# Optimization experiments

Measured on AMD Instinct MI355X. Metric: run time of the kernel, lower is better.

Reference implementation:

```python
import jax, jax.numpy as jnp
import numpy as np

C = 1024
HEADS = 8
HEAD_DIM = C // HEADS
SCALE = HEAD_DIM ** -0.5
GROUPS = 32
EPS = 1e-5


def _conv3(x, w, b):
    # 3x3x3 conv, padding=1 (SAME), NCDHW
    y = jax.lax.conv_general_dilated(x, w, (1, 1, 1), 'SAME',
                                     dimension_numbers=('NCDHW', 'OIDHW', 'NCDHW'))
    return y + b[None, :, None, None, None]


def _proj(x, w, b):
    # 1x1x1 conv == channel matmul; w: (C_out, C_in)
    return jnp.einsum('oc,bcdhw->bodhw', w, x) + b[None, :, None, None, None]


def _gn(x, g, b):
    B, Ch, D, H, W = x.shape
    xr = x.reshape(B, GROUPS, Ch // GROUPS, D, H, W)
    mu = xr.mean(axis=(2, 3, 4, 5), keepdims=True)
    var = xr.var(axis=(2, 3, 4, 5), keepdims=True)
    xn = ((xr - mu) * jax.lax.rsqrt(var + EPS)).reshape(B, Ch, D, H, W)
    return xn * g[None, :, None, None, None] + b[None, :, None, None, None]


def _attn(q, k, v):
    # q,k,v: (B,C,D,H,W) -> heads over channels, tokens over flattened spatial
    B, Ch, D, H, W = q.shape
    S = D * H * W
    q = q.reshape(B, HEADS, HEAD_DIM, S)
    k = k.reshape(B, HEADS, HEAD_DIM, S)
    v = v.reshape(B, HEADS, HEAD_DIM, S)
    logits = jnp.einsum('bhds,bhdt->bhst', q, k) * SCALE  # (B,H,S,S)
    a = jax.nn.softmax(logits, axis=-1)
    o = jnp.einsum('bhst,bhdt->bhds', a, v)
    return o.reshape(B, Ch, D, H, W)


def setup_inputs() -> dict:
    key = jax.random.key(0)
    ks = iter(jax.random.split(key, 40))
    def w(shape, s=0.02):
        return jax.random.normal(next(ks), shape, dtype=jnp.float32) * s
    B, D, H, W = 2, 8, 16, 16
    inp = {'x': jax.random.normal(next(ks), (B, C, D, H, W), dtype=jnp.float32)}
    for side in ('l', 'r'):
        inp[f'conv_{side}_w'] = w((C, C, 3, 3, 3))
        inp[f'conv_{side}_b'] = jnp.zeros((C,), jnp.float32)
        inp[f'gn_{side}_g'] = jnp.ones((C,), jnp.float32)
        inp[f'gn_{side}_b'] = jnp.zeros((C,), jnp.float32)
    for name in ('ql', 'kr', 'vr', 'qr', 'kl', 'vl'):
        inp[f'{name}_w'] = w((C, C))
        inp[f'{name}_b'] = jnp.zeros((C,), jnp.float32)
    inp['fus_w'] = w((C, C))
    inp['fus_b'] = jnp.zeros((C,), jnp.float32)
    inp['gn_f_g'] = jnp.ones((C,), jnp.float32)
    inp['gn_f_b'] = jnp.zeros((C,), jnp.float32)
    return inp


def reference(x, conv_l_w, conv_l_b, gn_l_g, gn_l_b,
              conv_r_w, conv_r_b, gn_r_g, gn_r_b,
              ql_w, ql_b, kr_w, kr_b, vr_w, vr_b,
              qr_w, qr_b, kl_w, kl_b, vl_w, vl_b,
              fus_w, fus_b, gn_f_g, gn_f_b):
    W = x.shape[-1]
    mid = W // 2
    x_left = x[..., :mid]
    x_right = x[..., mid:2 * mid]
    f_l = jax.nn.relu(_gn(_conv3(x_left, conv_l_w, conv_l_b), gn_l_g, gn_l_b))
    f_r = jax.nn.relu(_gn(_conv3(x_right, conv_r_w, conv_r_b), gn_r_g, gn_r_b))
    rf = jnp.flip(f_r, axis=-1)
    # left attends to flipped right
    out_l = _attn(_proj(f_l, ql_w, ql_b), _proj(rf, kr_w, kr_b), _proj(rf, vr_w, vr_b))
    # flipped right attends to left
    out_r = _attn(_proj(rf, qr_w, qr_b), _proj(f_l, kl_w, kl_b), _proj(f_l, vl_w, vl_b))
    asym_map = jnp.abs(f_l - rf).mean(axis=1, keepdims=True)
    out_r = jnp.flip(out_r, axis=-1)
    f_concat = jnp.concatenate([out_l, out_r], axis=-1)  # W even -> no pad needed
    fused = jax.nn.relu(_gn(_proj(f_concat, fus_w, fus_b), gn_f_g, gn_f_b))
    return fused, asym_map
```

## Files before the change

### kernel.cpp

```cpp
#include <hip/hip_runtime.h>
#include <hip/hip_bf16.h>
#include <stdint.h>


using bf16_t = __bf16;
using bf16x4 = __attribute__((ext_vector_type(4))) __bf16;
using bf16x8 = __attribute__((ext_vector_type(8))) __bf16;
using f32x4  = __attribute__((ext_vector_type(4))) float;

typedef const uint32_t __attribute__((address_space(1)))* gas1_t;
typedef uint32_t __attribute__((address_space(3)))* las3_t;

__device__ __forceinline__ f32x4 mfma16(bf16x8 a, bf16x8 b, f32x4 c) {
  return __builtin_amdgcn_mfma_f32_16x16x32_bf16(a, b, c, 0, 0, 0);
}
__device__ __forceinline__ void gload_lds16(const void* g, void* l) {
  __builtin_amdgcn_global_load_lds((gas1_t)g, (las3_t)l, 16, 0, 0);
}

__global__ __launch_bounds__(256) void convw_kernel(
    const float* __restrict__ wl, const float* __restrict__ wr,
    bf16_t* __restrict__ Wb)
{
  const int chunk = blockIdx.x;
  const int co    = blockIdx.y;
  const int side  = blockIdx.z;
  const float* __restrict__ src = (side ? wr : wl) + (size_t)co * 27648 + (size_t)chunk * 6912;
  __shared__ float L[6912];
  __shared__ bf16_t Lb[27][260];
  const int tid = threadIdx.x;
  for (int i = tid; i < 1728; i += 256)
    *(float4*)&L[i << 2] = *(const float4*)&src[i << 2];
  __syncthreads();
  {
    const int ci = tid;
#pragma unroll
    for (int t = 0; t < 27; ++t)
      Lb[t][ci] = (bf16_t)L[ci * 27 + t];
  }
  __syncthreads();
  bf16_t* __restrict__ dst = Wb + (size_t)side * (1024u * 27648u) + (size_t)co * 27648 + (chunk << 8);
  for (int u = tid; u < 864; u += 256) {
    const int t = u >> 5, c8 = (u & 31) << 3;
    const bf16x8 v = *(const bf16x8*)&Lb[t][c8];
    *(bf16x8*)&dst[(t << 10) + c8] = v;
  }
}

__global__ __launch_bounds__(256) void projw_kernel(
    const float* ql, const float* kl, const float* kr, const float* qr,
    const float* vl, const float* vr, const float* fu,
    bf16_t* __restrict__ Wp, float qs)
{
  const int z = blockIdx.y;
  const float* src; float s = 1.f;
  switch (z) {
    case 0: src = ql; s = qs; break;
    case 1: src = kl; break;
    case 2: src = kr; break;
    case 3: src = qr; s = qs; break;
    case 4: src = vl; break;
    case 5: src = vr; break;
    default: src = fu; break;
  }
  const size_t i4 = ((size_t)blockIdx.x * 256 + threadIdx.x) * 4;
  const float4 v = *(const float4*)(src + i4);
  bf16x4 o;
  o[0] = (bf16_t)(v.x * s); o[1] = (bf16_t)(v.y * s);
  o[2] = (bf16_t)(v.z * s); o[3] = (bf16_t)(v.w * s);
  *(bf16x4*)(Wp + (size_t)z * 1048576 + i4) = o;
}

__global__ __launch_bounds__(256) void xp_build_kernel(
    const float* __restrict__ x, bf16_t* __restrict__ Xp)
{
  const int cc0  = blockIdx.x << 6;
  const int d    = blockIdx.y;
  const int sb   = blockIdx.z;
  const int side = sb >> 1, b = sb & 1;
  __shared__ bf16_t Tls[64][132];
  const int tid = threadIdx.x;
#pragma unroll
  for (int j = 0; j < 8; ++j) {
    const int u = tid + (j << 8);
    const int ci = u >> 5, sub = u & 31;
    const int hh = sub >> 1, half = sub & 1;
    const float4 v = *(const float4*)&x[((size_t)((b << 10) + cc0 + ci) * 8 + d) * 256 +
                                        (hh << 4) + (side << 3) + (half << 2)];
    bf16x4 o;
    o[0] = (bf16_t)v.x; o[1] = (bf16_t)v.y; o[2] = (bf16_t)v.z; o[3] = (bf16_t)v.w;
    *(bf16x4*)&Tls[ci][(hh << 3) + (half << 2)] = o;
  }
  __syncthreads();
  bf16_t* __restrict__ dst = Xp + (size_t)side * 3686400 + (size_t)b * 1843200;
#pragma unroll
  for (int j = 0; j < 4; ++j) {
    const int u = tid + (j << 8);
    const int hw = u >> 3, c8 = u & 7;
    const int hh = hw >> 3, ww = hw & 7;
    bf16x8 v;
#pragma unroll
    for (int e = 0; e < 8; ++e) v[e] = Tls[(c8 << 3) + e][hw];
    *(bf16x8*)&dst[(size_t)(((d + 1) * 18 + (hh + 1)) * 10 + (ww + 1)) * 1024 + cc0 + (c8 << 3)] = v;
  }
}

#define STAGE_A(BUF, H, TILE)                                                 \
  { const int koff_ = t0k + (TILE) * 64;                                      \
    gload_lds16(A + (size_t)arow[H][0] * 27648 + koff_ + swz,                 \
                &Al[BUF][((H) * 128 + (wv << 4)) << 6]);                      \
    gload_lds16(A + (size_t)arow[H][1] * 27648 + koff_ + swz,                 \
                &Al[BUF][(((H) * 128 + (wv << 4)) + 8) << 6]); }

#define STAGE_B(BUF, H, TILE)                                                 \
  { const int t_ = t0 + ((TILE) >> 4);                                        \
    const int tofs_ = ((t_ / 9) * 18 + ((t_ / 3) % 3)) * 10 + (t_ % 3);       \
    const int cb64_ = ((TILE) & 15) << 6;                                     \
    gload_lds16(X + (size_t)(browbase[H][0] + tofs_) * 1024 + cb64_ + swz,    \
                &Bl[BUF][((H) * 128 + (wv << 4)) << 6]);                      \
    gload_lds16(X + (size_t)(browbase[H][1] + tofs_) * 1024 + cb64_ + swz,    \
                &Bl[BUF][(((H) * 128 + (wv << 4)) + 8) << 6]); }

#define READ_B(BUF)                                                           \
  _Pragma("unroll")                                                           \
  for (int n_ = 0; n_ < 4; ++n_) {                                            \
    const int row_ = (wn << 6) + (n_ << 4) + lane15;                          \
    const int c0_ = lane4 ^ (row_ & 7);                                       \
    const int c1_ = (4 + lane4) ^ (row_ & 7);                                 \
    b0[n_] = *(const bf16x8*)&Bl[BUF][(row_ << 6) + (c0_ << 3)];              \
    b1[n_] = *(const bf16x8*)&Bl[BUF][(row_ << 6) + (c1_ << 3)];              \
  }

#define READ_A(BUF, MBASE, D0, D1)                                           \
  _Pragma("unroll")                                                           \
  for (int m_ = 0; m_ < 4; ++m_) {                                            \
    const int row_ = (wm << 7) + (((MBASE) + m_) << 4) + lane15;              \
    const int c0_ = lane4 ^ (row_ & 7);                                       \
    const int c1_ = (4 + lane4) ^ (row_ & 7);                                 \
    D0[m_] = *(const bf16x8*)&Al[BUF][(row_ << 6) + (c0_ << 3)];              \
    D1[m_] = *(const bf16x8*)&Al[BUF][(row_ << 6) + (c1_ << 3)];              \
  }

#define MFMAQ(MBASE, AR, BR)                                                  \
  __builtin_amdgcn_s_setprio(1);                                              \
  _Pragma("unroll")                                                           \
  for (int m_ = 0; m_ < 4; ++m_)                                              \
    _Pragma("unroll")                                                         \
    for (int n_ = 0; n_ < 4; ++n_)                                            \
      acc[(MBASE) + m_][n_] = mfma16(AR[m_], BR[n_], acc[(MBASE) + m_][n_]);  \
  __builtin_amdgcn_s_setprio(0);

#define BAR __builtin_amdgcn_s_barrier()
#define LGKM0 asm volatile("s_waitcnt lgkmcnt(0)" ::: "memory")
#define VMC6 asm volatile("s_waitcnt vmcnt(6)" ::: "memory")
#define VMC0 asm volatile("s_waitcnt vmcnt(0)" ::: "memory")

__global__ __launch_bounds__(512, 2) void conv8_kernel(
    const bf16_t* __restrict__ Wb, const bf16_t* __restrict__ Xp,
    bf16_t* __restrict__ Pb)
{
  const int bid = blockIdx.x;
  const int orig = (bid & 7) * 32 + (bid >> 3);
  const int ntile = orig & 7;
  const int mtile = (orig >> 3) & 3;
  const int side  = (orig >> 5) & 1;
  const int slice = orig >> 6;
  const int t0 = slice * 7;
  const int t0k = t0 << 10;
  const int NTT = (slice == 3) ? 96 : 112;
  const int n0 = ntile << 8;
  const int m0 = mtile << 8;
  const int b = n0 >> 10;

  const bf16_t* __restrict__ A = Wb + (size_t)side * 28311552u;
  const bf16_t* __restrict__ X = Xp + (size_t)side * 3686400 + (size_t)b * 1843200;

  __shared__ bf16_t Al[2][256 * 64];
  __shared__ bf16_t Bl[2][256 * 64];

  const int tid = threadIdx.x;
  const int lane = tid & 63;
  const int wv = tid >> 6;
  const int wm = wv >> 2, wn = wv & 3;
  const int lane15 = lane & 15, lane4 = lane >> 4;
  const int l8 = lane >> 3, l7 = lane & 7;
  const int swz = (l7 ^ l8) << 3;

  int arow[2][2], browbase[2][2];
#pragma unroll
  for (int h = 0; h < 2; ++h)
#pragma unroll
    for (int j = 0; j < 2; ++j) {
      const int r = h * 128 + (wv << 4) + (j << 3) + l8;
      arow[h][j] = m0 + r;
      const int c = n0 + r;
      const int d = (c >> 7) & 7, hh = (c >> 3) & 15, ww = c & 7;
      browbase[h][j] = (d * 18 + hh) * 10 + ww;
    }

  const f32x4 fz = {0.f, 0.f, 0.f, 0.f};
  f32x4 acc[8][4];
#pragma unroll
  for (int i = 0; i < 8; ++i)
#pragma unroll
    for (int j = 0; j < 4; ++j) acc[i][j] = fz;
  bf16x8 b0[4], b1[4], a0k0[4], a0k1[4], a4k0[4], a4k1[4];

  STAGE_B(0, 0, 0)
  STAGE_B(0, 1, 0)
  STAGE_A(0, 0, 0)
  STAGE_A(0, 1, 0)
  STAGE_B(1, 0, 1)
  STAGE_B(1, 1, 1)
  STAGE_A(1, 0, 1)
  VMC6;
  BAR;

  const int NI = NTT >> 1;
  for (int i = 0; i < NI - 1; ++i) {
    const int tA = 2 * i + 1, tN0 = 2 * i + 2, tN1 = 2 * i + 3;
    READ_B(0) READ_A(0, 0, a0k0, a0k1)
    STAGE_A(1, 1, tA)
    BAR; LGKM0; MFMAQ(0, a0k0, b0) BAR;
    READ_A(0, 4, a4k0, a4k1)
    STAGE_B(0, 0, tN0)
    BAR; LGKM0; MFMAQ(4, a4k0, b0) BAR;
    STAGE_B(0, 1, tN0)
    BAR; MFMAQ(0, a0k1, b1) BAR;
    STAGE_A(0, 0, tN0)
    BAR; MFMAQ(4, a4k1, b1) VMC6; BAR;
    READ_B(1) READ_A(1, 0, a0k0, a0k1)
    STAGE_A(0, 1, tN0)
    BAR; LGKM0; MFMAQ(0, a0k0, b0) BAR;
    READ_A(1, 4, a4k0, a4k1)
    STAGE_B(1, 0, tN1)
    BAR; LGKM0; MFMAQ(4, a4k0, b0) BAR;
    STAGE_B(1, 1, tN1)
    BAR; MFMAQ(0, a0k1, b1) BAR;
    STAGE_A(1, 0, tN1)
    BAR; MFMAQ(4, a4k1, b1) VMC6; BAR;
  }
  {
    READ_B(0) READ_A(0, 0, a0k0, a0k1)
    STAGE_A(1, 1, NTT - 1)
    BAR; LGKM0; MFMAQ(0, a0k0, b0) BAR;
    READ_A(0, 4, a4k0, a4k1)
    BAR; LGKM0; MFMAQ(4, a4k0, b0) BAR;
    BAR; MFMAQ(0, a0k1, b1) BAR;
    BAR; MFMAQ(4, a4k1, b1) VMC0; BAR;
    READ_B(1) READ_A(1, 0, a0k0, a0k1)
    BAR; LGKM0; MFMAQ(0, a0k0, b0) BAR;
    READ_A(1, 4, a4k0, a4k1)
    BAR; LGKM0; MFMAQ(4, a4k0, b0) BAR;
    BAR; MFMAQ(0, a0k1, b1) BAR;
    BAR; MFMAQ(4, a4k1, b1) BAR;
  }

  bf16_t* __restrict__ P = Pb + (((size_t)(slice << 1) + side) << 21);
#pragma unroll
  for (int m = 0; m < 8; ++m) {
    const int row0 = m0 + (wm << 7) + (m << 4) + (lane4 << 2);
#pragma unroll
    for (int r = 0; r < 4; ++r) {
#pragma unroll
      for (int n = 0; n < 4; ++n) {
        const int col = n0 + (wn << 6) + (n << 4) + lane15;
        P[((size_t)(row0 + r) << 11) + col] = (bf16_t)acc[m][n][r];
      }
    }
  }
}

__global__ __launch_bounds__(256) void reduce4_kernel(
    const bf16_t* __restrict__ Pb, const float* __restrict__ bias_l,
    const float* __restrict__ bias_r, bf16_t* __restrict__ out_l, bf16_t* __restrict__ out_r,
    float* __restrict__ pS_lr, float* __restrict__ pQ_lr)
{
  const int id = blockIdx.x * 256 + threadIdx.x;
  const int tid = threadIdx.x;
  const int c8 = id & 255;
  const int co = (id >> 8) & 1023;
  const int side = id >> 18;
  const size_t off = ((size_t)co << 11) + ((size_t)c8 << 3);
  const float bia = (side ? bias_r : bias_l)[co];
  float acc[8];
#pragma unroll
  for (int e = 0; e < 8; ++e) acc[e] = bia;
#pragma unroll
  for (int s = 0; s < 4; ++s) {
    const bf16x8 v = *(const bf16x8*)&Pb[(((size_t)(s << 1) + side) << 21) + off];
#pragma unroll
    for (int e = 0; e < 8; ++e) acc[e] += (float)v[e];
  }
  bf16x8 ov;
#pragma unroll
  for (int e = 0; e < 8; ++e) ov[e] = (bf16_t)acc[e];
  *(bf16x8*)((side ? out_r : out_l) + off) = ov;
  float s = 0.f, q = 0.f;
#pragma unroll
  for (int e = 0; e < 8; ++e) { s += acc[e]; q += acc[e] * acc[e]; }
  __shared__ float sb[8];
  const int lane = tid & 63, wv = tid >> 6;
#pragma unroll
  for (int o = 1; o < 64; o <<= 1) { s += __shfl_xor(s, o, 64); q += __shfl_xor(q, o, 64); }
  if (lane == 0) { sb[wv] = s; sb[4 + wv] = q; }
  __syncthreads();
  if (tid == 0) {
    const int g = (side << 6) + (co >> 5);
    atomicAdd(&pS_lr[g],      sb[0] + sb[1]);
    atomicAdd(&pS_lr[g + 32], sb[2] + sb[3]);
    atomicAdd(&pQ_lr[g],      sb[4] + sb[5]);
    atomicAdd(&pQ_lr[g + 32], sb[6] + sb[7]);
  }
}

__device__ __forceinline__ void gemm_accum(
    const bf16_t* __restrict__ A, int lda,
    const bf16_t* __restrict__ Bt, int ldb,
    int K, f32x4 acc[4][4])
{
  __shared__ bf16_t Asm[128 * 64];
  __shared__ bf16_t Bsm[128 * 64];
  const int tid = threadIdx.x;
  const int lane = tid & 63;
  const int wv = tid >> 6;
  const int wm = wv >> 1, wn = wv & 1;
  const int lane15 = lane & 15, lane4 = lane >> 4;
  const int srow0 = (wv << 5) + (lane >> 3);
  const int sc = lane & 7;

  for (int k0 = 0; k0 < K; k0 += 64) {
#pragma unroll
    for (int i = 0; i < 4; ++i) {
      const int row = srow0 + (i << 3);
      gload_lds16(A + (size_t)row * lda + k0 + ((sc ^ (row & 7)) << 3),
                  &Asm[((wv << 2) + i) << 9]);
    }
#pragma unroll
    for (int i = 0; i < 4; ++i) {
      const int row = srow0 + (i << 3);
      gload_lds16(Bt + (size_t)row * ldb + k0 + ((sc ^ (row & 7)) << 3),
                  &Bsm[((wv << 2) + i) << 9]);
    }
    __syncthreads();
#pragma unroll
    for (int ks = 0; ks < 2; ++ks) {
      bf16x8 af[4];
#pragma unroll
      for (int mi = 0; mi < 4; ++mi) {
        const int row = (wm << 6) + (mi << 4) + lane15;
        const int ch = ((ks << 2) + lane4) ^ (row & 7);
        af[mi] = *(const bf16x8*)&Asm[(row << 6) + (ch << 3)];
      }
#pragma unroll
      for (int ni = 0; ni < 4; ++ni) {
        const int row = (wn << 6) + (ni << 4) + lane15;
        const int ch = ((ks << 2) + lane4) ^ (row & 7);
        const bf16x8 bfr = *(const bf16x8*)&Bsm[(row << 6) + (ch << 3)];
#pragma unroll
        for (int mi = 0; mi < 4; ++mi)
          acc[mi][ni] = mfma16(af[mi], bfr, acc[mi][ni]);
      }
    }
    __syncthreads();
  }
}

struct ProjTArgs {
  const bf16_t* act[2];
  const float*  bias[2][2];
  float         scl[2][2];
  bf16_t*       outp[2][2];
};
__global__ __launch_bounds__(256) void proj_t_kernel(const bf16_t* __restrict__ Wp, ProjTArgs a)
{
  const int side = blockIdx.z;
  const int n0 = blockIdx.x << 7;
  const int m0 = blockIdx.y << 7;
  const int seg = m0 >> 10;
  const f32x4 fz = {0.f, 0.f, 0.f, 0.f};
  f32x4 acc[4][4];
#pragma unroll
  for (int i = 0; i < 4; ++i)
#pragma unroll
    for (int j = 0; j < 4; ++j) acc[i][j] = fz;
  gemm_accum(a.act[side] + (size_t)n0 * 1024, 1024,
             Wp + (size_t)side * 2097152 + (size_t)m0 * 1024, 1024, 1024, acc);

  const int lane = threadIdx.x & 63, wv = threadIdx.x >> 6;
  const int wm = wv >> 1, wn = wv & 1;
  const int lane15 = lane & 15, lane4 = lane >> 4;
  const float* __restrict__ bias = a.bias[side][seg];
  const float bscale = a.scl[side][seg];
  bf16_t* __restrict__ C = a.outp[side][seg];
  const int mloc = (m0 & 1023) + (wn << 6);
  float bv[4];
#pragma unroll
  for (int ni = 0; ni < 4; ++ni) bv[ni] = bias[mloc + (ni << 4) + lane15] * bscale;
#pragma unroll
  for (int mi = 0; mi < 4; ++mi) {
    const int rowb = n0 + (wm << 6) + (mi << 4) + (lane4 << 2);
#pragma unroll
    for (int r = 0; r < 4; ++r) {
#pragma unroll
      for (int ni = 0; ni < 4; ++ni) {
        const int col = mloc + (ni << 4) + lane15;
        C[(size_t)(rowb + r) * 1024 + col] = (bf16_t)(acc[mi][ni][r] + bv[ni]);
      }
    }
  }
}

__global__ __launch_bounds__(256) void proj_v_kernel(
    const bf16_t* __restrict__ Wp, const bf16_t* __restrict__ flT,
    const bf16_t* __restrict__ rfT, const float* __restrict__ vlb,
    const float* __restrict__ vrb, bf16_t* __restrict__ Vl, bf16_t* __restrict__ Vr)
{
  const int side = blockIdx.z;
  const int m0 = blockIdx.x << 7;
  const int n0 = blockIdx.y << 7;
  const f32x4 fz = {0.f, 0.f, 0.f, 0.f};
  f32x4 acc[4][4];
#pragma unroll
  for (int i = 0; i < 4; ++i)
#pragma unroll
    for (int j = 0; j < 4; ++j) acc[i][j] = fz;
  gemm_accum(Wp + 4194304ull + (size_t)side * 1048576 + (size_t)m0 * 1024, 1024,
             (side ? rfT : flT) + (size_t)n0 * 1024, 1024, 1024, acc);

  const int lane = threadIdx.x & 63, wv = threadIdx.x >> 6;
  const int wm = wv >> 1, wn = wv & 1;
  const int lane15 = lane & 15, lane4 = lane >> 4;
  const float* __restrict__ bias = side ? vrb : vlb;
  bf16_t* __restrict__ C = side ? Vr : Vl;
#pragma unroll
  for (int mi = 0; mi < 4; ++mi) {
    const int row0 = m0 + (wm << 6) + (mi << 4) + (lane4 << 2);
#pragma unroll
    for (int r = 0; r < 4; ++r) {
      const float bia = bias[row0 + r];
#pragma unroll
      for (int ni = 0; ni < 4; ++ni) {
        const int col = n0 + (wn << 6) + (ni << 4) + lane15;
        C[(size_t)(row0 + r) * 2048 + col] = (bf16_t)(acc[mi][ni][r] + bia);
      }
    }
  }
}

__global__ __launch_bounds__(256) void fused_gemm_kernel(
    const bf16_t* __restrict__ Wf, const bf16_t* __restrict__ Bt, bf16_t* __restrict__ Pf)
{
  const int z = blockIdx.z;
  const int m0 = blockIdx.x << 7;
  const int n0 = blockIdx.y << 7;
  const f32x4 fz = {0.f, 0.f, 0.f, 0.f};
  f32x4 acc[4][4];
#pragma unroll
  for (int i = 0; i < 4; ++i)
#pragma unroll
    for (int j = 0; j < 4; ++j) acc[i][j] = fz;
  gemm_accum(Wf + (size_t)m0 * 1024 + (z << 9), 1024,
             Bt + (size_t)n0 * 1024 + (z << 9), 1024, 512, acc);

  const int lane = threadIdx.x & 63, wv = threadIdx.x >> 6;
  const int wm = wv >> 1, wn = wv & 1;
  const int lane15 = lane & 15, lane4 = lane >> 4;
  bf16_t* __restrict__ C = Pf + ((size_t)z << 22);
#pragma unroll
  for (int mi = 0; mi < 4; ++mi) {
    const int row0 = m0 + (wm << 6) + (mi << 4) + (lane4 << 2);
#pragma unroll
    for (int r = 0; r < 4; ++r) {
#pragma unroll
      for (int ni = 0; ni < 4; ++ni) {
        const int col = n0 + (wn << 6) + (ni << 4) + lane15;
        C[(size_t)(row0 + r) * 4096 + col] = (bf16_t)acc[mi][ni][r];
      }
    }
  }
}

__global__ __launch_bounds__(256) void gn_apply_lr_kernel(
    const bf16_t* __restrict__ yl, const bf16_t* __restrict__ yr,
    const float* __restrict__ gl, const float* __restrict__ bl,
    const float* __restrict__ gr, const float* __restrict__ br,
    const float* __restrict__ pS_lr, const float* __restrict__ pQ_lr,
    bf16_t* __restrict__ flT, bf16_t* __restrict__ rfT)
{
  const int side = blockIdx.z;
  const int n0 = blockIdx.x << 6;
  const int c0 = blockIdx.y << 6;
  const bf16_t* __restrict__ y = side ? yr : yl;
  const float* __restrict__ gamma = side ? gr : gl;
  const float* __restrict__ beta  = side ? br : bl;
  __shared__ float L[64][65];
  const int tid = threadIdx.x;
#pragma unroll
  for (int j = 0; j < 2; ++j) {
    const int u = tid + (j << 8);
    const int cr = u >> 3, ch = u & 7;
    const bf16x8 v = *(const bf16x8*)&y[(size_t)(c0 + cr) * 2048 + n0 + (ch << 3)];
#pragma unroll
    for (int e = 0; e < 8; ++e) L[cr][(ch << 3) + e] = (float)v[e];
  }
  __syncthreads();
  const int b = n0 >> 10;
  bf16_t* __restrict__ outT = side ? rfT : flT;
#pragma unroll
  for (int j = 0; j < 2; ++j) {
    const int u = tid + (j << 8);
    const int nr = u >> 3, c8 = u & 7;
    const int n = n0 + nr;
    const int nf = side ? ((n & ~7) | (7 - (n & 7))) : n;
    const int cbase = c0 + (c8 << 3);
    const int gidx = (side << 6) + (b << 5) + (cbase >> 5);
    const float m = pS_lr[gidx] * (1.f / 32768.f);
    const float rs = rsqrtf(pQ_lr[gidx] * (1.f / 32768.f) - m * m + 1e-5f);
    bf16x8 v;
#pragma unroll
    for (int e = 0; e < 8; ++e) {
      const int c = cbase + e;
      const float xv = (L[(c8 << 3) + e][nr] - m) * rs * gamma[c] + beta[c];
      v[e] = (bf16_t)fmaxf(xv, 0.f);
    }
    *(bf16x8*)&outT[(size_t)nf * 1024 + cbase] = v;
  }
}

__global__ __launch_bounds__(256, 2) void attn_kernel(
    const bf16_t* __restrict__ qlt, const bf16_t* __restrict__ krt, const bf16_t* __restrict__ vrm,
    const bf16_t* __restrict__ qrt, const bf16_t* __restrict__ klt, const bf16_t* __restrict__ vlm,
    bf16_t* __restrict__ xfc)
{
  const int st = blockIdx.x;
  const int bh = blockIdx.y;
  const int az = blockIdx.z;
  const int b = bh >> 3, h = bh & 7;
  const bf16_t* __restrict__ qt = az ? qrt : qlt;
  const bf16_t* __restrict__ kt = az ? klt : krt;
  const bf16_t* __restrict__ vm = az ? vlm : vrm;

  __shared__ bf16_t Ks[64 * 128];
  __shared__ bf16_t Vs[128 * 64];
  __shared__ bf16_t Ps[4][16 * 64];

  const int tid = threadIdx.x, lane = tid & 63, wv = tid >> 6;
  const int lane15 = lane & 15, lane4 = lane >> 4;

  bf16x8 qf[4];
  {
    const bf16_t* __restrict__ qbase = qt + (size_t)((b << 10) + (st << 6)) * 1024 + (h << 7);
    const int row = (wv << 4) + lane15;
#pragma unroll
    for (int kk = 0; kk < 4; ++kk)
      qf[kk] = *(const bf16x8*)&qbase[(size_t)row * 1024 + (kk << 5) + (lane4 << 3)];
  }

  const f32x4 fz = {0.f, 0.f, 0.f, 0.f};
  f32x4 oacc[8];
#pragma unroll
  for (int nj = 0; nj < 8; ++nj) oacc[nj] = fz;
  float mrun[4], lrun[4];
#pragma unroll
  for (int r = 0; r < 4; ++r) { mrun[r] = -3.0e38f; lrun[r] = 0.f; }

  for (int it = 0; it < 16; ++it) {
    __syncthreads();
#pragma unroll
    for (int j = 0; j < 4; ++j) {
      const int g = (wv << 2) + j;
      const int row = (g << 2) + lane4;
      gload_lds16(kt + (size_t)((b << 10) + (it << 6) + row) * 1024 + (h << 7) + ((lane15 ^ (row & 7)) << 3),
                  &Ks[g << 9]);
    }
#pragma unroll
    for (int j = 0; j < 4; ++j) {
      const int g = (wv << 2) + j;
      const int row = (g << 3) + (lane >> 3);
      gload_lds16(vm + (size_t)((h << 7) + row) * 2048 + (b << 10) + (it << 6) + (((lane & 7) ^ (row & 7)) << 3),
                  &Vs[g << 9]);
    }
    __syncthreads();
    f32x4 la[4];
#pragma unroll
    for (int tj = 0; tj < 4; ++tj) la[tj] = fz;
#pragma unroll
    for (int kk = 0; kk < 4; ++kk) {
#pragma unroll
      for (int tj = 0; tj < 4; ++tj) {
        const int row = (tj << 4) + lane15;
        const int ch = ((kk << 2) + lane4) ^ (row & 7);
        const bf16x8 kf = *(const bf16x8*)&Ks[(row << 7) + (ch << 3)];
        la[tj] = mfma16(qf[kk], kf, la[tj]);
      }
    }
    float mx[4];
    int ok = 1;
#pragma unroll
    for (int r = 0; r < 4; ++r) {
      float m_ = la[0][r];
#pragma unroll
      for (int tj = 1; tj < 4; ++tj) m_ = fmaxf(m_, la[tj][r]);
#pragma unroll
      for (int o = 1; o < 16; o <<= 1) m_ = fmaxf(m_, __shfl_xor(m_, o, 64));
      mx[r] = m_;
      ok &= (m_ <= mrun[r] + 8.f) ? 1 : 0;
    }
    if (!__all(ok)) {
#pragma unroll
      for (int r = 0; r < 4; ++r) {
        const float mnew = fmaxf(mrun[r], mx[r]);
        const float alpha = __builtin_amdgcn_exp2f(mrun[r] - mnew);
        mrun[r] = mnew;
        lrun[r] *= alpha;
#pragma unroll
        for (int nj = 0; nj < 8; ++nj) oacc[nj][r] *= alpha;
      }
    }
#pragma unroll
    for (int r = 0; r < 4; ++r) {
      const int row = (lane4 << 2) + r;
      float rs = 0.f;
#pragma unroll
      for (int tj = 0; tj < 4; ++tj) {
        const float p = __builtin_amdgcn_exp2f(la[tj][r] - mrun[r]);
        rs += p;
        const int byte_ = ((tj << 5) + (lane15 << 1)) ^ ((row & 7) << 4);
        *(bf16_t*)((char*)(&Ps[wv][0]) + (row << 7) + byte_) = (bf16_t)p;
      }
#pragma unroll
      for (int o = 1; o < 16; o <<= 1) rs += __shfl_xor(rs, o, 64);
      lrun[r] += rs;
    }
#pragma unroll
    for (int kk = 0; kk < 2; ++kk) {
      const int prow = lane15;
      const int pch = ((kk << 2) + lane4) ^ (prow & 7);
      const bf16x8 pf = *(const bf16x8*)&Ps[wv][(prow << 6) + (pch << 3)];
#pragma unroll
      for (int nj = 0; nj < 8; ++nj) {
        const int row = (nj << 4) + lane15;
        const int ch = ((kk << 2) + lane4) ^ (row & 7);
        const bf16x8 vf = *(const bf16x8*)&Vs[(row << 6) + (ch << 3)];
        oacc[nj] = mfma16(pf, vf, oacc[nj]);
      }
    }
  }
#pragma unroll
  for (int r = 0; r < 4; ++r) {
    const int sl = (wv << 4) + (lane4 << 2) + r;
    const int s = (st << 6) + sl;
    const int dd = s >> 7, hh2 = (s >> 3) & 15, ww = s & 7;
    const int w16 = az ? (15 - ww) : ww;
    const int n16 = (b << 11) + ((dd << 4) + hh2) * 16 + w16;
    const float inv = 1.f / lrun[r];
#pragma unroll
    for (int nj = 0; nj < 8; ++nj) {
      const int c = (h << 7) + (nj << 4) + lane15;
      xfc[(size_t)n16 * 1024 + c] = (bf16_t)(oacc[nj][r] * inv);
    }
  }
}

__global__ __launch_bounds__(256) void gn_partial_f_kernel(
    const bf16_t* __restrict__ Pf, const float* __restrict__ bias,
    float* __restrict__ pS, float* __restrict__ pQ)
{
  const int bg = blockIdx.x;
  const int sl = blockIdx.y;
  const int b = bg >> 5, g = bg & 31;
  const int tid = threadIdx.x;
  const int c = (g << 5) + (tid >> 3);
  const int s0 = (sl << 8) + ((tid & 7) << 5);
  const size_t base = (size_t)c * 4096 + (b << 11) + s0;
  const float bia = bias[c];
  float s = 0.f, q = 0.f;
#pragma unroll
  for (int u = 0; u < 4; ++u) {
    const bf16x8 v0 = *(const bf16x8*)&Pf[base + (u << 3)];
    const bf16x8 v1 = *(const bf16x8*)&Pf[base + (u << 3) + 4194304];
#pragma unroll
    for (int e = 0; e < 8; ++e) {
      const float v = (float)v0[e] + (float)v1[e] + bia;
      s += v; q += v * v;
    }
  }
  __shared__ float sb[8];
  const int lane = tid & 63, wv = tid >> 6;
#pragma unroll
  for (int o = 1; o < 64; o <<= 1) { s += __shfl_xor(s, o, 64); q += __shfl_xor(q, o, 64); }
  if (lane == 0) { sb[wv] = s; sb[4 + wv] = q; }
  __syncthreads();
  if (tid == 0) {
    pS[(bg << 3) + sl] = sb[0] + sb[1] + sb[2] + sb[3];
    pQ[(bg << 3) + sl] = sb[4] + sb[5] + sb[6] + sb[7];
  }
}

__global__ __launch_bounds__(256) void gn_apply_f_kernel(
    const bf16_t* __restrict__ Pf, const float* __restrict__ bias,
    const float* __restrict__ gamma, const float* __restrict__ beta,
    const float* __restrict__ pS, const float* __restrict__ pQ,
    float* __restrict__ outp)
{
  const int id = blockIdx.x * 256 + threadIdx.x;
  const int s8 = id & 255;
  const int c = (id >> 8) & 1023;
  const int b = id >> 18;
  const int gidx = (b << 5) + (c >> 5);
  float S = 0.f, Q = 0.f;
#pragma unroll
  for (int sl = 0; sl < 8; ++sl) { S += pS[(gidx << 3) + sl]; Q += pQ[(gidx << 3) + sl]; }
  const float m = S * (1.f / 65536.f);
  const float rs = rsqrtf(Q * (1.f / 65536.f) - m * m + 1e-5f);
  const float gm = gamma[c], bt = beta[c], bia = bias[c];
  const size_t idx = (size_t)c * 4096 + (b << 11) + (s8 << 3);
  const bf16x8 v0 = *(const bf16x8*)&Pf[idx];
  const bf16x8 v1 = *(const bf16x8*)&Pf[idx + 4194304];
  float o[8];
#pragma unroll
  for (int e = 0; e < 8; ++e) {
    const float v = (float)v0[e] + (float)v1[e] + bia;
    o[e] = fmaxf((v - m) * rs * gm + bt, 0.f);
  }
  float* __restrict__ op = &outp[(((size_t)(b << 10) + c) << 11) + (s8 << 3)];
  float4 o0, o1;
  o0.x = o[0]; o0.y = o[1]; o0.z = o[2]; o0.w = o[3];
  o1.x = o[4]; o1.y = o[5]; o1.z = o[6]; o1.w = o[7];
  *(float4*)op = o0;
  *(float4*)(op + 4) = o1;
}

__global__ __launch_bounds__(256) void asym_kernel(
    const bf16_t* __restrict__ flT, const bf16_t* __restrict__ rfT, float* __restrict__ outp)
{
  const int n = blockIdx.x;
  const int tid = threadIdx.x;
  const bf16x4 a = *(const bf16x4*)&flT[(size_t)n * 1024 + (tid << 2)];
  const bf16x4 c = *(const bf16x4*)&rfT[(size_t)n * 1024 + (tid << 2)];
  float s = 0.f;
#pragma unroll
  for (int e = 0; e < 4; ++e) s += fabsf((float)a[e] - (float)c[e]);
  __shared__ float sb[4];
  const int lane = tid & 63, wv = tid >> 6;
#pragma unroll
  for (int o = 1; o < 64; o <<= 1) s += __shfl_xor(s, o, 64);
  if (lane == 0) sb[wv] = s;
  __syncthreads();
  if (tid == 0) outp[n] = (sb[0] + sb[1] + sb[2] + sb[3]) * (1.f / 1024.f);
}

extern "C" void kernel_launch(void* const* d_in, const int* in_sizes, int n_in,
                              void* d_out, int out_size, void* d_ws, size_t ws_size,
                              hipStream_t stream)
{
  (void)in_sizes; (void)n_in; (void)out_size; (void)ws_size;
  const float* x    = (const float*)d_in[0];
  const float* clw  = (const float*)d_in[1];
  const float* clb  = (const float*)d_in[2];
  const float* glg  = (const float*)d_in[3];
  const float* glb_ = (const float*)d_in[4];
  const float* crw  = (const float*)d_in[5];
  const float* crb  = (const float*)d_in[6];
  const float* grg  = (const float*)d_in[7];
  const float* grb  = (const float*)d_in[8];
  const float* qlw = (const float*)d_in[9];  const float* qlb = (const float*)d_in[10];
  const float* krw = (const float*)d_in[11]; const float* krb = (const float*)d_in[12];
  const float* vrw = (const float*)d_in[13]; const float* vrb = (const float*)d_in[14];
  const float* qrw = (const float*)d_in[15]; const float* qrb = (const float*)d_in[16];
  const float* klw = (const float*)d_in[17]; const float* klb = (const float*)d_in[18];
  const float* vlw = (const float*)d_in[19]; const float* vlb = (const float*)d_in[20];
  const float* fuw = (const float*)d_in[21]; const float* fub = (const float*)d_in[22];
  const float* gfg = (const float*)d_in[23]; const float* gfb = (const float*)d_in[24];
  float* out = (float*)d_out;

  char* ws = (char*)d_ws;
  size_t off = 0;
  auto take = [&](size_t bytes) -> char* {
    char* p = ws + off; off += (bytes + 255) & ~(size_t)255; return p;
  };
  bf16_t* Wb    = (bf16_t*)take(113246208ull);
  bf16_t* Wp    = (bf16_t*)take(14680064ull);
  bf16_t* Xp    = (bf16_t*)take(14745600ull);
  float*  pS_lr = (float*) take(512);
  float*  pQ_lr = (float*) take(512);
  bf16_t* convL = (bf16_t*)take(4194304ull);
  bf16_t* convR = (bf16_t*)take(4194304ull);
  bf16_t* flT   = (bf16_t*)take(4194304ull);
  bf16_t* rfT   = (bf16_t*)take(4194304ull);
  float*  pS    = (float*) take(2048);
  float*  pQ    = (float*) take(2048);
  bf16_t* Pb    = (bf16_t*)take(33554432ull);

  char* al = (char*)Wb; size_t aoff = 0;
  auto takeA = [&](size_t bytes) -> char* {
    char* p = al + aoff; aoff += (bytes + 255) & ~(size_t)255; return p;
  };
  bf16_t* qlT = (bf16_t*)takeA(4194304ull);
  bf16_t* klT = (bf16_t*)takeA(4194304ull);
  bf16_t* krT = (bf16_t*)takeA(4194304ull);
  bf16_t* qrT = (bf16_t*)takeA(4194304ull);
  bf16_t* Vl  = (bf16_t*)takeA(4194304ull);
  bf16_t* Vr  = (bf16_t*)takeA(4194304ull);
  bf16_t* xfcT = (bf16_t*)takeA(8388608ull);
  bf16_t* Pf   = (bf16_t*)takeA(16777216ull);

  const float QS = 0.08838834764831843f * 1.4426950408889634f;

  hipMemsetAsync(Xp, 0, 14745600ull + 1024ull, stream);
  convw_kernel<<<dim3(4, 1024, 2), 256, 0, stream>>>(clw, crw, Wb);
  projw_kernel<<<dim3(1024, 7), 256, 0, stream>>>(qlw, klw, krw, qrw, vlw, vrw, fuw, Wp, QS);
  xp_build_kernel<<<dim3(16, 8, 4), 256, 0, stream>>>(x, Xp);
  conv8_kernel<<<dim3(256), 512, 0, stream>>>(Wb, Xp, Pb);
  reduce4_kernel<<<dim3(2048), 256, 0, stream>>>(Pb, clb, crb, convL, convR, pS_lr, pQ_lr);
  gn_apply_lr_kernel<<<dim3(32, 16, 2), 256, 0, stream>>>(convL, convR, glg, glb_, grg, grb,
                                                          pS_lr, pQ_lr, flT, rfT);
  ProjTArgs pa;
  pa.act[0] = flT; pa.act[1] = rfT;
  pa.bias[0][0] = qlb; pa.bias[0][1] = klb;
  pa.bias[1][0] = krb; pa.bias[1][1] = qrb;
  pa.scl[0][0] = QS;  pa.scl[0][1] = 1.f;
  pa.scl[1][0] = 1.f; pa.scl[1][1] = QS;
  pa.outp[0][0] = qlT; pa.outp[0][1] = klT;
  pa.outp[1][0] = krT; pa.outp[1][1] = qrT;
  proj_t_kernel<<<dim3(16, 16, 2), 256, 0, stream>>>(Wp, pa);
  proj_v_kernel<<<dim3(8, 16, 2), 256, 0, stream>>>(Wp, flT, rfT, vlb, vrb, Vl, Vr);

  attn_kernel<<<dim3(16, 16, 2), 256, 0, stream>>>(qlT, krT, Vr, qrT, klT, Vl, xfcT);
  fused_gemm_kernel<<<dim3(8, 32, 2), 256, 0, stream>>>(Wp + 6ull * 1048576, xfcT, Pf);
  gn_partial_f_kernel<<<dim3(64, 8), 256, 0, stream>>>(Pf, fub, pS, pQ);
  gn_apply_f_kernel<<<dim3(2048), 256, 0, stream>>>(Pf, fub, gfg, gfb, pS, pQ, out);
  asym_kernel<<<dim3(2048), 256, 0, stream>>>(flT, rfT, out + 4194304);
}
```

Measured before the change: 441.7 us.

## Rebalance conv K-split evenly and shrink register fragments with finer LDS reads

Each of the four K-slices now covers exactly 108 tiles instead of 112/112/112/96, so the blocks carry equal work. The A and B fragment reads are split into per-k-step loads, which cuts the A fragment registers from four arrays to one and reorders the global-to-LDS staging (vmcnt 4 instead of 6). This is meant to relieve register pressure and even out the tail. The cost is an LDS-read-plus-wait before every MFMA quad, which adds latency exposure.

```diff
diff --git a/kernel.cpp b/kernel.cpp
--- a/kernel.cpp
+++ b/kernel.cpp
@@ -106,14 +106,14 @@
 }
 
 #define STAGE_A(BUF, H, TILE)                                                 \
-  { const int koff_ = t0k + (TILE) * 64;                                      \
+  { const int koff_ = (TILE) << 6;                                            \
     gload_lds16(A + (size_t)arow[H][0] * 27648 + koff_ + swz,                 \
                 &Al[BUF][((H) * 128 + (wv << 4)) << 6]);                      \
     gload_lds16(A + (size_t)arow[H][1] * 27648 + koff_ + swz,                 \
                 &Al[BUF][(((H) * 128 + (wv << 4)) + 8) << 6]); }
 
 #define STAGE_B(BUF, H, TILE)                                                 \
-  { const int t_ = t0 + ((TILE) >> 4);                                        \
+  { const int t_ = (TILE) >> 4;                                               \
     const int tofs_ = ((t_ / 9) * 18 + ((t_ / 3) % 3)) * 10 + (t_ % 3);       \
     const int cb64_ = ((TILE) & 15) << 6;                                     \
     gload_lds16(X + (size_t)(browbase[H][0] + tofs_) * 1024 + cb64_ + swz,    \
@@ -121,38 +121,42 @@
     gload_lds16(X + (size_t)(browbase[H][1] + tofs_) * 1024 + cb64_ + swz,    \
                 &Bl[BUF][(((H) * 128 + (wv << 4)) + 8) << 6]); }
 
-#define READ_B(BUF)                                                           \
+#define READ_B0(BUF)                                                          \
   _Pragma("unroll")                                                           \
   for (int n_ = 0; n_ < 4; ++n_) {                                            \
     const int row_ = (wn << 6) + (n_ << 4) + lane15;                          \
-    const int c0_ = lane4 ^ (row_ & 7);                                       \
-    const int c1_ = (4 + lane4) ^ (row_ & 7);                                 \
-    b0[n_] = *(const bf16x8*)&Bl[BUF][(row_ << 6) + (c0_ << 3)];              \
-    b1[n_] = *(const bf16x8*)&Bl[BUF][(row_ << 6) + (c1_ << 3)];              \
-  }
-
-#define READ_A(BUF, MBASE, D0, D1)                                           \
+    const int c_ = lane4 ^ (row_ & 7);                                        \
+    b0[n_] = *(const bf16x8*)&Bl[BUF][(row_ << 6) + (c_ << 3)];               \
+  }
+
+#define READ_B1(BUF)                                                          \
+  _Pragma("unroll")                                                           \
+  for (int n_ = 0; n_ < 4; ++n_) {                                            \
+    const int row_ = (wn << 6) + (n_ << 4) + lane15;                          \
+    const int c_ = (4 + lane4) ^ (row_ & 7);                                  \
+    b1[n_] = *(const bf16x8*)&Bl[BUF][(row_ << 6) + (c_ << 3)];               \
+  }
+
+#define READ_A(BUF, MBASE, KS)                                                \
   _Pragma("unroll")                                                           \
   for (int m_ = 0; m_ < 4; ++m_) {                                            \
     const int row_ = (wm << 7) + (((MBASE) + m_) << 4) + lane15;              \
-    const int c0_ = lane4 ^ (row_ & 7);                                       \
-    const int c1_ = (4 + lane4) ^ (row_ & 7);                                 \
-    D0[m_] = *(const bf16x8*)&Al[BUF][(row_ << 6) + (c0_ << 3)];              \
-    D1[m_] = *(const bf16x8*)&Al[BUF][(row_ << 6) + (c1_ << 3)];              \
-  }
-
-#define MFMAQ(MBASE, AR, BR)                                                  \
+    const int c_ = (((KS) << 2) + lane4) ^ (row_ & 7);                        \
+    a[m_] = *(const bf16x8*)&Al[BUF][(row_ << 6) + (c_ << 3)];                \
+  }
+
+#define MFMAQ(MBASE, BR)                                                      \
   __builtin_amdgcn_s_setprio(1);                                              \
   _Pragma("unroll")                                                           \
   for (int m_ = 0; m_ < 4; ++m_)                                              \
     _Pragma("unroll")                                                         \
     for (int n_ = 0; n_ < 4; ++n_)                                            \
-      acc[(MBASE) + m_][n_] = mfma16(AR[m_], BR[n_], acc[(MBASE) + m_][n_]);  \
+      acc[(MBASE) + m_][n_] = mfma16(a[m_], BR[n_], acc[(MBASE) + m_][n_]);   \
   __builtin_amdgcn_s_setprio(0);
 
 #define BAR __builtin_amdgcn_s_barrier()
 #define LGKM0 asm volatile("s_waitcnt lgkmcnt(0)" ::: "memory")
-#define VMC6 asm volatile("s_waitcnt vmcnt(6)" ::: "memory")
+#define VMC4 asm volatile("s_waitcnt vmcnt(4)" ::: "memory")
 #define VMC0 asm volatile("s_waitcnt vmcnt(0)" ::: "memory")
 
 __global__ __launch_bounds__(512, 2) void conv8_kernel(
@@ -165,9 +169,7 @@
   const int mtile = (orig >> 3) & 3;
   const int side  = (orig >> 5) & 1;
   const int slice = orig >> 6;
-  const int t0 = slice * 7;
-  const int t0k = t0 << 10;
-  const int NTT = (slice == 3) ? 96 : 112;
+  const int tb = slice * 108;
   const int n0 = ntile << 8;
   const int m0 = mtile << 8;
   const int b = n0 >> 10;
@@ -204,56 +206,64 @@
   for (int i = 0; i < 8; ++i)
 #pragma unroll
     for (int j = 0; j < 4; ++j) acc[i][j] = fz;
-  bf16x8 b0[4], b1[4], a0k0[4], a0k1[4], a4k0[4], a4k1[4];
-
-  STAGE_B(0, 0, 0)
-  STAGE_B(0, 1, 0)
-  STAGE_A(0, 0, 0)
-  STAGE_A(0, 1, 0)
-  STAGE_B(1, 0, 1)
-  STAGE_B(1, 1, 1)
-  STAGE_A(1, 0, 1)
-  VMC6;
+  bf16x8 b0[4], b1[4], a[4];
+
+  STAGE_B(0, 0, tb)
+  STAGE_B(0, 1, tb)
+  STAGE_A(0, 0, tb)
+  STAGE_A(0, 1, tb)
+  STAGE_B(1, 0, tb + 1)
+  STAGE_B(1, 1, tb + 1)
+  VMC4;
   BAR;
 
-  const int NI = NTT >> 1;
-  for (int i = 0; i < NI - 1; ++i) {
-    const int tA = 2 * i + 1, tN0 = 2 * i + 2, tN1 = 2 * i + 3;
-    READ_B(0) READ_A(0, 0, a0k0, a0k1)
-    STAGE_A(1, 1, tA)
-    BAR; LGKM0; MFMAQ(0, a0k0, b0) BAR;
-    READ_A(0, 4, a4k0, a4k1)
-    STAGE_B(0, 0, tN0)
-    BAR; LGKM0; MFMAQ(4, a4k0, b0) BAR;
-    STAGE_B(0, 1, tN0)
-    BAR; MFMAQ(0, a0k1, b1) BAR;
-    STAGE_A(0, 0, tN0)
-    BAR; MFMAQ(4, a4k1, b1) VMC6; BAR;
-    READ_B(1) READ_A(1, 0, a0k0, a0k1)
-    STAGE_A(0, 1, tN0)
-    BAR; LGKM0; MFMAQ(0, a0k0, b0) BAR;
-    READ_A(1, 4, a4k0, a4k1)
-    STAGE_B(1, 0, tN1)
-    BAR; LGKM0; MFMAQ(4, a4k0, b0) BAR;
-    STAGE_B(1, 1, tN1)
-    BAR; MFMAQ(0, a0k1, b1) BAR;
-    STAGE_A(1, 0, tN1)
-    BAR; MFMAQ(4, a4k1, b1) VMC6; BAR;
+  for (int i = 0; i < 53; ++i) {
+    const int T1 = tb + 2 * i + 1, T2 = tb + 2 * i + 2, T3 = tb + 2 * i + 3;
+    READ_B0(0) READ_A(0, 0, 0)
+    STAGE_A(1, 0, T1)
+    BAR; LGKM0; MFMAQ(0, b0) BAR;
+    READ_B1(0) READ_A(0, 4, 0)
+    STAGE_A(1, 1, T1)
+    BAR; LGKM0; MFMAQ(4, b0) BAR;
+    READ_A(0, 0, 1)
+    STAGE_B(0, 0, T2)
+    BAR; LGKM0; MFMAQ(0, b1) BAR;
+    READ_A(0, 4, 1)
+    STAGE_B(0, 1, T2)
+    BAR; LGKM0; MFMAQ(4, b1) VMC4; BAR;
+    READ_B0(1) READ_A(1, 0, 0)
+    STAGE_A(0, 0, T2)
+    BAR; LGKM0; MFMAQ(0, b0) BAR;
+    READ_B1(1) READ_A(1, 4, 0)
+    STAGE_A(0, 1, T2)
+    BAR; LGKM0; MFMAQ(4, b0) BAR;
+    READ_A(1, 0, 1)
+    STAGE_B(1, 0, T3)
+    BAR; LGKM0; MFMAQ(0, b1) BAR;
+    READ_A(1, 4, 1)
+    STAGE_B(1, 1, T3)
+    BAR; LGKM0; MFMAQ(4, b1) VMC4; BAR;
   }
   {
-    READ_B(0) READ_A(0, 0, a0k0, a0k1)
-    STAGE_A(1, 1, NTT - 1)
-    BAR; LGKM0; MFMAQ(0, a0k0, b0) BAR;
-    READ_A(0, 4, a4k0, a4k1)
-    BAR; LGKM0; MFMAQ(4, a4k0, b0) BAR;
-    BAR; MFMAQ(0, a0k1, b1) BAR;
-    BAR; MFMAQ(4, a4k1, b1) VMC0; BAR;
-    READ_B(1) READ_A(1, 0, a0k0, a0k1)
-    BAR; LGKM0; MFMAQ(0, a0k0, b0) BAR;
-    READ_A(1, 4, a4k0, a4k1)
-    BAR; LGKM0; MFMAQ(4, a4k0, b0) BAR;
-    BAR; MFMAQ(0, a0k1, b1) BAR;
-    BAR; MFMAQ(4, a4k1, b1) BAR;
+    const int T1 = tb + 107;
+    READ_B0(0) READ_A(0, 0, 0)
+    STAGE_A(1, 0, T1)
+    BAR; LGKM0; MFMAQ(0, b0) BAR;
+    READ_B1(0) READ_A(0, 4, 0)
+    STAGE_A(1, 1, T1)
+    BAR; LGKM0; MFMAQ(4, b0) BAR;
+    READ_A(0, 0, 1)
+    BAR; LGKM0; MFMAQ(0, b1) BAR;
+    READ_A(0, 4, 1)
+    BAR; LGKM0; MFMAQ(4, b1) VMC0; BAR;
+    READ_B0(1) READ_A(1, 0, 0)
+    BAR; LGKM0; MFMAQ(0, b0) BAR;
+    READ_B1(1) READ_A(1, 4, 0)
+    BAR; LGKM0; MFMAQ(4, b0) BAR;
+    READ_A(1, 0, 1)
+    BAR; LGKM0; MFMAQ(0, b1) BAR;
+    READ_A(1, 4, 1)
+    BAR; LGKM0; MFMAQ(4, b1) BAR;
   }
 
   bf16_t* __restrict__ P = Pb + (((size_t)(slice << 1) + side) << 21);
```

Measured after the change: 488.7 us. 1.11x slower.
